# Kernel tuning notes

Measured on AMD Instinct MI355X. Metric: run time of the kernel, lower is better.

The kernel has to match this reference:

```python
import jax, jax.numpy as jnp
import numpy as np

B, S, D = 4, 1024, 512          # batch, seq, d_model
F, DF = 16, 64                  # raw feature dim, d_feat_emb
E, H = 8, 1024                  # n_experts (4 groups x scale 2), expert hidden
DFF = 2048                      # shared FFN hidden = max(round(d_ff*1.0), d_model)
K = 2                           # top_k
TEMP = 1.0                      # router temperature
EPS = 1e-5                      # layer_norm_eps


def _ln(x, g, b):
    m = jnp.mean(x, axis=-1, keepdims=True)
    v = jnp.mean(jnp.square(x - m), axis=-1, keepdims=True)
    return (x - m) * jax.lax.rsqrt(v + EPS) * g + b


def setup_inputs() -> dict:
    key = jax.random.key(0)
    ks = jax.random.split(key, 16)

    def w(k, shape, fan_in):
        return jax.random.normal(k, shape, dtype=jnp.float32) * (1.0 / np.sqrt(fan_in))

    return {
        "hidden_states": jax.random.normal(ks[0], (B, S, D), dtype=jnp.float32),
        "stage_raw_feat": jax.random.normal(ks[1], (B, S, F), dtype=jnp.float32),
        "ln_g": jnp.ones((D,), jnp.float32),
        "ln_b": jnp.zeros((D,), jnp.float32),
        "pre_ln_g": jnp.ones((D,), jnp.float32),
        "pre_ln_b": jnp.zeros((D,), jnp.float32),
        "feat_w": w(ks[2], (F, DF), F),
        "feat_b": jnp.zeros((DF,), jnp.float32),
        "film_w": w(ks[3], (DF, 2 * D), DF),
        "film_b": jnp.zeros((2 * D,), jnp.float32),
        "router_w": w(ks[4], (D, E), D),
        "router_b": jnp.zeros((E,), jnp.float32),
        "w1": w(ks[5], (E, D, H), D),
        "b1": jnp.zeros((E, H), jnp.float32),
        "w2": w(ks[6], (E, H, D), H),
        "b2": jnp.zeros((E, D), jnp.float32),
        "fc1_w": w(ks[7], (D, DFF), D),
        "fc1_b": jnp.zeros((DFF,), jnp.float32),
        "fc2_w": w(ks[8], (DFF, D), DFF),
        "fc2_b": jnp.zeros((D,), jnp.float32),
        "alpha": jnp.float32(0.5),
    }


def reference(hidden_states, stage_raw_feat, ln_g, ln_b, pre_ln_g, pre_ln_b,
              feat_w, feat_b, film_w, film_b, router_w, router_b,
              w1, b1, w2, b2, fc1_w, fc1_b, fc2_w, fc2_b, alpha):
    # Pre-MoE LayerNorm
    x = _ln(hidden_states, ln_g, ln_b)                       # [B,S,D]

    # Feature encoder + FiLM injection of stage features into expert input
    feat = stage_raw_feat @ feat_w + feat_b                  # [B,S,DF]
    film = feat @ film_w + film_b                            # [B,S,2D]
    gamma, beta = jnp.split(film, 2, axis=-1)
    x_in = x * (1.0 + gamma) + beta                          # [B,S,D]

    # Token-level learned router (source='hidden'), top-k softmax over picked logits
    logits = (x @ router_w + router_b) / TEMP                # [B,S,E]
    top_vals, top_idx = jax.lax.top_k(logits, K)             # [B,S,K]
    gates = jax.nn.softmax(top_vals, axis=-1)                # [B,S,K]
    gate_full = (jax.nn.one_hot(top_idx, E, dtype=x.dtype) * gates[..., None]).sum(-2)  # [B,S,E]

    # Expert MLPs (depth=1): dense all-expert compute, sparse gate combine
    h = jax.nn.gelu(jnp.einsum('bsd,edh->bseh', x_in, w1) + b1)          # [B,S,E,H]
    moe = jnp.einsum('bseh,ehd,bse->bsd', h, w2, gate_full)
    moe = moe + jnp.einsum('bse,ed->bsd', gate_full, b2)                 # [B,S,D]

    # Shared FFN residual branch (shared_moe_learned)
    xs = _ln(hidden_states, pre_ln_g, pre_ln_b)
    shared = jax.nn.gelu(xs @ fc1_w + fc1_b) @ fc2_w + fc2_b             # [B,S,D]

    return hidden_states + shared + alpha * moe
```

## Files before the change

### kernel.cpp

```cpp
#include <hip/hip_runtime.h>
#include <hip/hip_bf16.h>

typedef __attribute__((ext_vector_type(8))) short short8;
typedef __attribute__((ext_vector_type(4))) float f32x4;
typedef unsigned short u16;

#define TTOK 4096
#define DMOD 512
#define DFFN 2048
#define NEXP 8
#define HEXP 1024

__device__ __forceinline__ u16 to_bf16(float f) {
    union { __hip_bfloat16 h; u16 u; } cv;
    cv.h = __float2bfloat16(f);
    return cv.u;
}

__device__ __forceinline__ float gelu_tanh(float x) {
    const float c = 0.7978845608028654f;
    float y = c * (x + 0.044715f * x * x * x);
    return x / (1.0f + __expf(-2.0f * y));
}

__device__ __forceinline__ float4 ld_bf4(const u16* p) {
    ushort4 u = *(const ushort4*)p;
    union { unsigned i; float f; } a, b, c, d;
    a.i = (unsigned)u.x << 16; b.i = (unsigned)u.y << 16;
    c.i = (unsigned)u.z << 16; d.i = (unsigned)u.w << 16;
    return make_float4(a.f, b.f, c.f, d.f);
}

__device__ __forceinline__ void gload16(const u16* g, u16* l) {
    __builtin_amdgcn_global_load_lds(
        (__attribute__((address_space(1))) void*)g,
        (__attribute__((address_space(3))) void*)l, 16, 0, 0);
}

__global__ __launch_bounds__(256) void pack_weights(
    const float* __restrict__ fc1_w, const float* __restrict__ fc2_w,
    const float* __restrict__ w1, const float* __restrict__ w2,
    u16* __restrict__ fc1p, u16* __restrict__ fc2p,
    u16* __restrict__ w1p, u16* __restrict__ w2p)
{
    int t = blockIdx.x * 256 + threadIdx.x;
    const float* src; u16* dst; int N, k, n;
    if (t < 131072) {
        int u = t; int lane = u & 63; int fs = u >> 6; int s = fs & 15;
        int q = lane >> 4, rr = lane & 15;
        src = fc1_w; dst = fc1p + (size_t)u * 8; N = 2048;
        k = s * 32 + q * 8; n = ((fs >> 4) * 16) + rr;
    } else if (t < 262144) {
        int u = t - 131072; int lane = u & 63; int fs = u >> 6; int s = fs & 63;
        int q = lane >> 4, rr = lane & 15;
        src = fc2_w; dst = fc2p + (size_t)u * 8; N = 512;
        k = s * 32 + q * 8; n = ((fs >> 6) * 16) + rr;
    } else if (t < 786432) {
        int u = t - 262144; int e = u >> 16; int v = u & 65535;
        int lane = v & 63; int fs = v >> 6; int s = fs & 15;
        int q = lane >> 4, rr = lane & 15;
        src = w1 + (size_t)e * 524288; dst = w1p + (size_t)u * 8; N = 1024;
        k = s * 32 + q * 8; n = ((fs >> 4) * 16) + rr;
    } else {
        int u = t - 786432; int e = u >> 16; int v = u & 65535;
        int lane = v & 63; int fs = v >> 6; int s = fs & 31;
        int q = lane >> 4, rr = lane & 15;
        src = w2 + (size_t)e * 524288; dst = w2p + (size_t)u * 8; N = 512;
        k = s * 32 + q * 8; n = ((fs >> 5) * 16) + rr;
    }
    u16 ov[8];
#pragma unroll
    for (int j = 0; j < 8; ++j)
        ov[j] = to_bf16(src[(size_t)(k + j) * N + n]);
    *(uint4*)dst = *(uint4*)ov;
}

__global__ __launch_bounds__(256) void ln_kernel(
    const float* __restrict__ hidden, const float* __restrict__ raw,
    const float* __restrict__ ln_g, const float* __restrict__ ln_b,
    const float* __restrict__ pre_g, const float* __restrict__ pre_b,
    const float* __restrict__ feat_w, const float* __restrict__ feat_b,
    const float* __restrict__ router_w, const float* __restrict__ router_b,
    u16* __restrict__ xs, float* __restrict__ xbuf, float* __restrict__ featbuf,
    float* __restrict__ logits)
{
    const int tid = threadIdx.x, lane = tid & 63, w = tid >> 6;
    const int t = blockIdx.x * 4 + w;
    __shared__ float pl8[4][64][8];
    __shared__ float raw_sh[4][16];

    const float* xrow = hidden + (size_t)t * DMOD + lane * 8;
    float4 xa = *(const float4*)(xrow);
    float4 xb = *(const float4*)(xrow + 4);
    if (lane < 16) raw_sh[w][lane] = raw[(size_t)t * 16 + lane];

    float s = xa.x + xa.y + xa.z + xa.w + xb.x + xb.y + xb.z + xb.w;
    float q = xa.x*xa.x + xa.y*xa.y + xa.z*xa.z + xa.w*xa.w
            + xb.x*xb.x + xb.y*xb.y + xb.z*xb.z + xb.w*xb.w;
#pragma unroll
    for (int m = 32; m > 0; m >>= 1) { s += __shfl_xor(s, m); q += __shfl_xor(q, m); }
    float mean = s * (1.0f / 512.0f);
    float var  = q * (1.0f / 512.0f) - mean * mean;
    float rstd = rsqrtf(var + 1e-5f);

    float4 na, nb;
    na.x = (xa.x - mean) * rstd; na.y = (xa.y - mean) * rstd;
    na.z = (xa.z - mean) * rstd; na.w = (xa.w - mean) * rstd;
    nb.x = (xb.x - mean) * rstd; nb.y = (xb.y - mean) * rstd;
    nb.z = (xb.z - mean) * rstd; nb.w = (xb.w - mean) * rstd;

    const int d8 = lane * 8;
    float4 pga = *(const float4*)(pre_g + d8), pgb = *(const float4*)(pre_g + d8 + 4);
    float4 pba = *(const float4*)(pre_b + d8), pbb = *(const float4*)(pre_b + d8 + 4);
    u16 ov[8];
    ov[0] = to_bf16(na.x * pga.x + pba.x); ov[1] = to_bf16(na.y * pga.y + pba.y);
    ov[2] = to_bf16(na.z * pga.z + pba.z); ov[3] = to_bf16(na.w * pga.w + pba.w);
    ov[4] = to_bf16(nb.x * pgb.x + pbb.x); ov[5] = to_bf16(nb.y * pgb.y + pbb.y);
    ov[6] = to_bf16(nb.z * pgb.z + pbb.z); ov[7] = to_bf16(nb.w * pgb.w + pbb.w);
    *(uint4*)(xs + (size_t)t * DMOD + d8) = *(uint4*)ov;

    float4 lga = *(const float4*)(ln_g + d8), lgb = *(const float4*)(ln_g + d8 + 4);
    float4 lba = *(const float4*)(ln_b + d8), lbb = *(const float4*)(ln_b + d8 + 4);
    float4 x03, x47;
    x03.x = na.x * lga.x + lba.x; x03.y = na.y * lga.y + lba.y;
    x03.z = na.z * lga.z + lba.z; x03.w = na.w * lga.w + lba.w;
    x47.x = nb.x * lgb.x + lbb.x; x47.y = nb.y * lgb.y + lbb.y;
    x47.z = nb.z * lgb.z + lbb.z; x47.w = nb.w * lgb.w + lbb.w;
    *(float4*)(xbuf + (size_t)t * DMOD + d8) = x03;
    *(float4*)(xbuf + (size_t)t * DMOD + d8 + 4) = x47;

    float4 p03 = make_float4(0.f, 0.f, 0.f, 0.f), p47 = p03;
    const float* rw = router_w + (size_t)d8 * 8;
#pragma unroll
    for (int j = 0; j < 8; ++j) {
        float xv = (j < 4) ? ((j == 0) ? x03.x : (j == 1) ? x03.y : (j == 2) ? x03.z : x03.w)
                           : ((j == 4) ? x47.x : (j == 5) ? x47.y : (j == 6) ? x47.z : x47.w);
        float4 r0 = *(const float4*)(rw + j * 8);
        float4 r1 = *(const float4*)(rw + j * 8 + 4);
        p03.x += xv * r0.x; p03.y += xv * r0.y; p03.z += xv * r0.z; p03.w += xv * r0.w;
        p47.x += xv * r1.x; p47.y += xv * r1.y; p47.z += xv * r1.z; p47.w += xv * r1.w;
    }
    *(float4*)(&pl8[w][lane][0]) = p03;
    *(float4*)(&pl8[w][lane][4]) = p47;
    if (lane < 8) {
        float acc = router_b[lane];
#pragma unroll 8
        for (int i = 0; i < 64; ++i) acc += pl8[w][i][lane];
        logits[(size_t)t * 8 + lane] = acc;
    }

    float fv = feat_b[lane];
#pragma unroll
    for (int f = 0; f < 16; ++f) fv += raw_sh[w][f] * feat_w[f * 64 + lane];
    featbuf[(size_t)t * 64 + lane] = fv;
}

__global__ __launch_bounds__(256) void bucket_kernel(
    const float* __restrict__ logits, int* __restrict__ cnt, int* __restrict__ slots,
    float* __restrict__ gslot, int* __restrict__ eslot)
{
    const int tid = threadIdx.x;
    const int t = blockIdx.x * 256 + tid;
    __shared__ int csh[8], base[8];
    if (tid < 8) csh[tid] = 0;
    __syncthreads();

    float4 l0 = *(const float4*)(logits + (size_t)t * 8);
    float4 l1 = *(const float4*)(logits + (size_t)t * 8 + 4);
    float v0 = -1e30f, v1 = -1e30f; int i0 = 0, i1 = 0;
#define CK(val, idx) { float v = (val); if (v > v0) { v1 = v0; i1 = i0; v0 = v; i0 = idx; } \
                       else if (v > v1) { v1 = v; i1 = idx; } }
    CK(l0.x, 0) CK(l0.y, 1) CK(l0.z, 2) CK(l0.w, 3)
    CK(l1.x, 4) CK(l1.y, 5) CK(l1.z, 6) CK(l1.w, 7)
#undef CK
    float g1 = 1.0f / (1.0f + __expf(v0 - v1));
    float g0 = 1.0f - g1;
    int r0 = atomicAdd(&csh[i0], 1);
    int r1 = atomicAdd(&csh[i1], 1);
    __syncthreads();
    if (tid < 8) base[tid] = atomicAdd(&cnt[tid], csh[tid]);
    __syncthreads();
    int p0 = base[i0] + r0, p1 = base[i1] + r1;
    slots[i0 * TTOK + p0] = 2 * t;
    slots[i1 * TTOK + p1] = 2 * t + 1;
    gslot[2 * t] = g0;     eslot[2 * t] = i0;
    gslot[2 * t + 1] = g1; eslot[2 * t + 1] = i1;
}

__global__ __launch_bounds__(256) void film_kernel(
    const float* __restrict__ xbuf, const float* __restrict__ featbuf,
    const float* __restrict__ film_w, const float* __restrict__ film_b,
    u16* __restrict__ xin)
{
    const int t0 = blockIdx.x * 8, tid = threadIdx.x;
    __shared__ float fs[8 * 64];
#pragma unroll
    for (int i = 0; i < 2; ++i)
        fs[tid + i * 256] = featbuf[(size_t)t0 * 64 + tid + i * 256];
    __syncthreads();

    float acc[8][4];
#pragma unroll
    for (int t = 0; t < 8; ++t) { acc[t][0] = 0.f; acc[t][1] = 0.f; acc[t][2] = 0.f; acc[t][3] = 0.f; }

    for (int j = 0; j < 64; ++j) {
        const float* fw = film_w + (size_t)j * 1024 + tid;
        float w0 = fw[0], w1 = fw[256], w2 = fw[512], w3 = fw[768];
#pragma unroll
        for (int t = 0; t < 8; ++t) {
            float fv = fs[t * 64 + j];
            acc[t][0] += fv * w0; acc[t][1] += fv * w1;
            acc[t][2] += fv * w2; acc[t][3] += fv * w3;
        }
    }
    float b0 = film_b[tid], b1 = film_b[tid + 256], b2 = film_b[tid + 512], b3 = film_b[tid + 768];
#pragma unroll
    for (int t = 0; t < 8; ++t) {
        size_t row = (size_t)(t0 + t) * DMOD;
        float xv0 = xbuf[row + tid], xv1 = xbuf[row + tid + 256];
        xin[row + tid]       = to_bf16(xv0 * (1.0f + acc[t][0] + b0) + acc[t][2] + b2);
        xin[row + tid + 256] = to_bf16(xv1 * (1.0f + acc[t][1] + b1) + acc[t][3] + b3);
    }
}

template<int KCHUNKS>
__device__ __forceinline__ void gemm32(
    const u16* const rp[8],
    const u16* Bf0, int S, int sbase,
    f32x4 acc[2][4], u16* As)
{
    const int tid = threadIdx.x, lane = tid & 63, w = tid >> 6;
    const int q = lane >> 4, rr = lane & 15, l7 = lane & 7;
#pragma unroll
    for (int mi = 0; mi < 2; ++mi)
#pragma unroll
        for (int nj = 0; nj < 4; ++nj) {
            acc[mi][nj][0] = 0.f; acc[mi][nj][1] = 0.f;
            acc[mi][nj][2] = 0.f; acc[mi][nj][3] = 0.f;
        }
    const u16* Bi[4];
#pragma unroll
    for (int i = 0; i < 4; ++i)
        Bi[i] = Bf0 + ((size_t)i * S + sbase) * 512 + lane * 8;

#pragma unroll
    for (int i = 0; i < 8; ++i)
        gload16(rp[i] + (lane ^ i) * 8, As + (w * 8 + i) * 512);
    __syncthreads();

    short8 bn[4];
#pragma unroll
    for (int i = 0; i < 4; ++i) bn[i] = *(const short8*)(Bi[i]);

    const int a0base = rr * 512, a1base = (16 + rr) * 512;
#pragma unroll
    for (int c = 0; c < KCHUNKS; ++c) {
#pragma unroll
        for (int sl = 0; sl < 16; ++sl) {
            short8 b0 = bn[0], b1 = bn[1], b2 = bn[2], b3 = bn[3];
            int nstep = c * 16 + sl + 1;
            if (nstep < KCHUNKS * 16) {
#pragma unroll
                for (int i = 0; i < 4; ++i)
                    bn[i] = *(const short8*)(Bi[i] + (size_t)nstep * 512);
            }
            int pa = ((sl * 4 + q) ^ l7) * 8;
            short8 a0 = *(const short8*)(As + a0base + pa);
            short8 a1 = *(const short8*)(As + a1base + pa);
            acc[0][0] = __builtin_amdgcn_mfma_f32_16x16x32_bf16(a0, b0, acc[0][0], 0, 0, 0);
            acc[1][0] = __builtin_amdgcn_mfma_f32_16x16x32_bf16(a1, b0, acc[1][0], 0, 0, 0);
            acc[0][1] = __builtin_amdgcn_mfma_f32_16x16x32_bf16(a0, b1, acc[0][1], 0, 0, 0);
            acc[1][1] = __builtin_amdgcn_mfma_f32_16x16x32_bf16(a1, b1, acc[1][1], 0, 0, 0);
            acc[0][2] = __builtin_amdgcn_mfma_f32_16x16x32_bf16(a0, b2, acc[0][2], 0, 0, 0);
            acc[1][2] = __builtin_amdgcn_mfma_f32_16x16x32_bf16(a1, b2, acc[1][2], 0, 0, 0);
            acc[0][3] = __builtin_amdgcn_mfma_f32_16x16x32_bf16(a0, b3, acc[0][3], 0, 0, 0);
            acc[1][3] = __builtin_amdgcn_mfma_f32_16x16x32_bf16(a1, b3, acc[1][3], 0, 0, 0);
        }
        if (c + 1 < KCHUNKS) {
            __syncthreads();
#pragma unroll
            for (int i = 0; i < 8; ++i)
                gload16(rp[i] + (c + 1) * 512 + (lane ^ i) * 8, As + (w * 8 + i) * 512);
            __syncthreads();
        }
    }
}

__global__ __launch_bounds__(256) void stage1_kernel(
    const u16* __restrict__ xs, const u16* __restrict__ fc1p, const float* __restrict__ fc1_b,
    u16* __restrict__ h1,
    const u16* __restrict__ xin, const u16* __restrict__ w1p, const float* __restrict__ b1,
    const int* __restrict__ cnt, const int* __restrict__ slots, u16* __restrict__ hbuf)
{
    __shared__ __align__(16) u16 As[16384];
    const int tid = threadIdx.x, lane = tid & 63, w = tid >> 6;
    const int cb = lane & 15, rq = (lane >> 4) * 4;
    const int m0 = blockIdx.x * 32;
    const u16* rp[8];
    f32x4 acc[2][4];

    if (blockIdx.z == 8) {
        const int f0 = blockIdx.y * 16 + w * 4;
#pragma unroll
        for (int i = 0; i < 8; ++i) rp[i] = xs + (size_t)(m0 + w * 8 + i) * 512;
        gemm32<1>(rp, fc1p + (size_t)f0 * 8192, 16, 0, acc, As);
#pragma unroll
        for (int mi = 0; mi < 2; ++mi)
#pragma unroll
            for (int nj = 0; nj < 4; ++nj) {
                int col = (f0 + nj) * 16 + cb;
                float bias = fc1_b[col];
#pragma unroll
                for (int r = 0; r < 4; ++r) {
                    int row = m0 + mi * 16 + rq + r;
                    h1[(size_t)row * DFFN + col] = to_bf16(gelu_tanh(acc[mi][nj][r] + bias));
                }
            }
    } else {
        if (blockIdx.y >= 4) return;
        const int e = blockIdx.z, ce = cnt[e];
        if (m0 >= ce) return;
        const int* sl = slots + e * TTOK;
        const int f0 = blockIdx.y * 16 + w * 4;
#pragma unroll
        for (int i = 0; i < 8; ++i) {
            int p = m0 + w * 8 + i; if (p > ce - 1) p = ce - 1;
            rp[i] = xin + (size_t)(sl[p] >> 1) * 512;
        }
        gemm32<1>(rp, w1p + (size_t)e * 524288 + (size_t)f0 * 8192, 16, 0, acc, As);
#pragma unroll
        for (int mi = 0; mi < 2; ++mi)
#pragma unroll
            for (int r = 0; r < 4; ++r) {
                int p = m0 + mi * 16 + rq + r;
                if (p < ce) {
                    int slot = sl[p];
#pragma unroll
                    for (int nj = 0; nj < 4; ++nj) {
                        int col = (f0 + nj) * 16 + cb;
                        hbuf[(size_t)slot * HEXP + col] = to_bf16(gelu_tanh(acc[mi][nj][r] + b1[e * HEXP + col]));
                    }
                }
            }
    }
}

__global__ __launch_bounds__(256) void stage2_kernel(
    const u16* __restrict__ h1, const u16* __restrict__ fc2p,
    const u16* __restrict__ hbuf, const u16* __restrict__ w2p,
    const int* __restrict__ cnt, const int* __restrict__ slots,
    u16* __restrict__ pf, u16* __restrict__ pm)
{
    __shared__ __align__(16) u16 As[16384];
    const int tid = threadIdx.x, lane = tid & 63, w = tid >> 6;
    const int cb = lane & 15, rq = (lane >> 4) * 4;
    const int m0 = blockIdx.x * 32;
    const int ks = blockIdx.y & 1, nb = blockIdx.y >> 1;
    const int f0 = nb * 16 + w * 4;
    const u16* rp[8];
    f32x4 acc[2][4];

    if (blockIdx.z == 8) {
#pragma unroll
        for (int i = 0; i < 8; ++i)
            rp[i] = h1 + (size_t)(m0 + w * 8 + i) * DFFN + ks * 1024;
        gemm32<2>(rp, fc2p + (size_t)f0 * 32768, 64, ks * 32, acc, As);
        u16* dst = pf + (size_t)ks * TTOK * DMOD;
#pragma unroll
        for (int mi = 0; mi < 2; ++mi)
#pragma unroll
            for (int nj = 0; nj < 4; ++nj) {
                int col = (f0 + nj) * 16 + cb;
#pragma unroll
                for (int r = 0; r < 4; ++r) {
                    int row = m0 + mi * 16 + rq + r;
                    dst[(size_t)row * DMOD + col] = to_bf16(acc[mi][nj][r]);
                }
            }
    } else {
        const int e = blockIdx.z, ce = cnt[e];
        if (m0 >= ce) return;
        const int* sl = slots + e * TTOK;
#pragma unroll
        for (int i = 0; i < 8; ++i) {
            int p = m0 + w * 8 + i; if (p > ce - 1) p = ce - 1;
            rp[i] = hbuf + (size_t)sl[p] * HEXP + ks * 512;
        }
        gemm32<1>(rp, w2p + (size_t)e * 524288 + (size_t)f0 * 16384, 32, ks * 16, acc, As);
        u16* dst = pm + (size_t)ks * 2 * TTOK * DMOD;
#pragma unroll
        for (int mi = 0; mi < 2; ++mi)
#pragma unroll
            for (int r = 0; r < 4; ++r) {
                int p = m0 + mi * 16 + rq + r;
                if (p < ce) {
                    int slot = sl[p];
#pragma unroll
                    for (int nj = 0; nj < 4; ++nj) {
                        int col = (f0 + nj) * 16 + cb;
                        dst[(size_t)slot * DMOD + col] = to_bf16(acc[mi][nj][r]);
                    }
                }
            }
    }
}

__global__ __launch_bounds__(256) void combine_kernel(
    const float* __restrict__ hidden, const u16* __restrict__ pf, const u16* __restrict__ pm,
    const float* __restrict__ fc2_b, const float* __restrict__ b2,
    const float* __restrict__ gslot, const int* __restrict__ eslot,
    const float* __restrict__ alpha, float* __restrict__ out)
{
    int i = blockIdx.x * 256 + threadIdx.x;
    int t = i >> 7, d = (i & 127) * 4;
    float a = alpha[0];
    float4 h = ((const float4*)hidden)[i];
    float4 bias = *(const float4*)(fc2_b + d);

    size_t fo = (size_t)t * DMOD + d;
    float4 f0 = ld_bf4(pf + fo), f1 = ld_bf4(pf + (size_t)TTOK * DMOD + fo);

    int s0 = 2 * t, s1 = 2 * t + 1;
    float g0 = gslot[s0], g1 = gslot[s1];
    int e0 = eslot[s0], e1 = eslot[s1];
    size_t mo0 = (size_t)s0 * DMOD + d, mo1 = (size_t)s1 * DMOD + d;
    const u16* pm1 = pm + (size_t)2 * TTOK * DMOD;
    float4 ma = ld_bf4(pm + mo0), mb = ld_bf4(pm1 + mo0);
    float4 mc = ld_bf4(pm + mo1), md = ld_bf4(pm1 + mo1);
    float4 ba = *(const float4*)(b2 + e0 * DMOD + d);
    float4 bb = *(const float4*)(b2 + e1 * DMOD + d);

    float4 o;
    o.x = h.x + f0.x + f1.x + bias.x + a * (g0 * (ma.x + mb.x + ba.x) + g1 * (mc.x + md.x + bb.x));
    o.y = h.y + f0.y + f1.y + bias.y + a * (g0 * (ma.y + mb.y + ba.y) + g1 * (mc.y + md.y + bb.y));
    o.z = h.z + f0.z + f1.z + bias.z + a * (g0 * (ma.z + mb.z + ba.z) + g1 * (mc.z + md.z + bb.z));
    o.w = h.w + f0.w + f1.w + bias.w + a * (g0 * (ma.w + mb.w + ba.w) + g1 * (mc.w + md.w + bb.w));
    ((float4*)out)[i] = o;
}

extern "C" void kernel_launch(void* const* d_in, const int* in_sizes, int n_in,
                              void* d_out, int out_size, void* d_ws, size_t ws_size,
                              hipStream_t stream)
{
    const float* hidden   = (const float*)d_in[0];
    const float* raw      = (const float*)d_in[1];
    const float* ln_g     = (const float*)d_in[2];
    const float* ln_b     = (const float*)d_in[3];
    const float* pre_g    = (const float*)d_in[4];
    const float* pre_b    = (const float*)d_in[5];
    const float* feat_w   = (const float*)d_in[6];
    const float* feat_b   = (const float*)d_in[7];
    const float* film_w   = (const float*)d_in[8];
    const float* film_b   = (const float*)d_in[9];
    const float* router_w = (const float*)d_in[10];
    const float* router_b = (const float*)d_in[11];
    const float* w1       = (const float*)d_in[12];
    const float* b1       = (const float*)d_in[13];
    const float* w2       = (const float*)d_in[14];
    const float* b2       = (const float*)d_in[15];
    const float* fc1_w    = (const float*)d_in[16];
    const float* fc1_b    = (const float*)d_in[17];
    const float* fc2_w    = (const float*)d_in[18];
    const float* fc2_b    = (const float*)d_in[19];
    const float* alpha    = (const float*)d_in[20];
    float* out = (float*)d_out;

    char* w = (char*)d_ws;
    auto alloc = [&](size_t b) { char* p = w; w += (b + 255) & ~(size_t)255; return p; };
    u16*  fc1p = (u16*)alloc((size_t)DFFN * DMOD * 2);
    u16*  fc2p = (u16*)alloc((size_t)DMOD * DFFN * 2);
    u16*  w1p  = (u16*)alloc((size_t)NEXP * HEXP * DMOD * 2);
    u16*  w2p  = (u16*)alloc((size_t)NEXP * DMOD * HEXP * 2);
    u16*  xs   = (u16*)alloc((size_t)TTOK * DMOD * 2);
    u16*  xin  = (u16*)alloc((size_t)TTOK * DMOD * 2);
    u16*  h1   = (u16*)alloc((size_t)TTOK * DFFN * 2);
    u16*  hb   = (u16*)alloc((size_t)2 * TTOK * HEXP * 2);
    u16*  pf   = (u16*)alloc((size_t)2 * TTOK * DMOD * 2);
    u16*  pm   = (u16*)alloc((size_t)2 * 2 * TTOK * DMOD * 2);
    int*   cnt   = (int*)alloc(NEXP * 4);
    int*   slots = (int*)alloc((size_t)NEXP * TTOK * 4);
    float* gslot = (float*)alloc((size_t)2 * TTOK * 4);
    int*   eslot = (int*)alloc((size_t)2 * TTOK * 4);
    float* logits = (float*)alloc((size_t)TTOK * 8 * 4);
    float* xbuf  = (float*)pm;
    float* featbuf = (float*)h1;

    hipMemsetAsync(cnt, 0, NEXP * 4, stream);
    pack_weights<<<5120, 256, 0, stream>>>(fc1_w, fc2_w, w1, w2, fc1p, fc2p, w1p, w2p);
    ln_kernel<<<1024, 256, 0, stream>>>(hidden, raw, ln_g, ln_b, pre_g, pre_b,
        feat_w, feat_b, router_w, router_b, xs, xbuf, featbuf, logits);
    bucket_kernel<<<16, 256, 0, stream>>>(logits, cnt, slots, gslot, eslot);
    film_kernel<<<512, 256, 0, stream>>>(xbuf, featbuf, film_w, film_b, xin);
    stage1_kernel<<<dim3(128, 8, 9), 256, 0, stream>>>(xs, fc1p, fc1_b, h1,
        xin, w1p, b1, cnt, slots, hb);
    stage2_kernel<<<dim3(128, 4, 9), 256, 0, stream>>>(h1, fc2p, hb, w2p, cnt, slots, pf, pm);
    combine_kernel<<<2048, 256, 0, stream>>>(hidden, pf, pm, fc2_b, b2, gslot, eslot, alpha, out);
}
```

Before: 252.5 us.

## Enlarge GEMM M-tile to 64 rows with double-buffered B fragments

Replaces the 32-row GEMM tile with a 64-row tile, so each block does 16 MFMAs per step and every B fragment loaded from global memory is reused across four A sub-tiles instead of two. A is now staged in 256-wide K chunks with a new XOR swizzle that is applied in the global load addresses, and B fragments are prefetched two steps ahead in a ping-pong register buffer. The grid's M dimension is halved to match. This cuts weight traffic per output but raises register pressure from 64 accumulator floats and yields fewer blocks, so occupancy and tail efficiency may drop, especially for sparse experts.

```diff
diff --git a/kernel.cpp b/kernel.cpp
--- a/kernel.cpp
+++ b/kernel.cpp
@@ -223,64 +223,78 @@
     }
 }
 
-template<int KCHUNKS>
-__device__ __forceinline__ void gemm32(
+template<int NSTEPS>
+__device__ __forceinline__ void gemm64(
     const u16* const rp[8],
     const u16* Bf0, int S, int sbase,
-    f32x4 acc[2][4], u16* As)
+    f32x4 acc[4][4], u16* As)
 {
     const int tid = threadIdx.x, lane = tid & 63, w = tid >> 6;
-    const int q = lane >> 4, rr = lane & 15, l7 = lane & 7;
-#pragma unroll
-    for (int mi = 0; mi < 2; ++mi)
+    const int q = lane >> 4, rr = lane & 15;
+#pragma unroll
+    for (int mi = 0; mi < 4; ++mi)
 #pragma unroll
         for (int nj = 0; nj < 4; ++nj) {
             acc[mi][nj][0] = 0.f; acc[mi][nj][1] = 0.f;
             acc[mi][nj][2] = 0.f; acc[mi][nj][3] = 0.f;
         }
-    const u16* Bi[4];
+    const u16* Bn[4];
 #pragma unroll
     for (int i = 0; i < 4; ++i)
-        Bi[i] = Bf0 + ((size_t)i * S + sbase) * 512 + lane * 8;
-
-#pragma unroll
-    for (int i = 0; i < 8; ++i)
-        gload16(rp[i] + (lane ^ i) * 8, As + (w * 8 + i) * 512);
+        Bn[i] = Bf0 + ((size_t)i * S + sbase) * 512 + lane * 8;
+
+#pragma unroll
+    for (int j = 0; j < 8; ++j)
+        gload16(rp[j], As + (w * 16 + 2 * j) * 256);
+
+    short8 bb[2][4];
+#pragma unroll
+    for (int i = 0; i < 4; ++i) { bb[0][i] = *(const short8*)(Bn[i]); }
+#pragma unroll
+    for (int i = 0; i < 4; ++i) { bb[1][i] = *(const short8*)(Bn[i] + 512); Bn[i] += 1024; }
     __syncthreads();
 
-    short8 bn[4];
-#pragma unroll
-    for (int i = 0; i < 4; ++i) bn[i] = *(const short8*)(Bi[i]);
-
-    const int a0base = rr * 512, a1base = (16 + rr) * 512;
-#pragma unroll
-    for (int c = 0; c < KCHUNKS; ++c) {
-#pragma unroll
-        for (int sl = 0; sl < 16; ++sl) {
-            short8 b0 = bn[0], b1 = bn[1], b2 = bn[2], b3 = bn[3];
-            int nstep = c * 16 + sl + 1;
-            if (nstep < KCHUNKS * 16) {
-#pragma unroll
-                for (int i = 0; i < 4; ++i)
-                    bn[i] = *(const short8*)(Bi[i] + (size_t)nstep * 512);
+    constexpr int NCH = NSTEPS / 8;
+    const int ab0 = rr * 256, ab1 = (16 + rr) * 256, ab2 = (32 + rr) * 256, ab3 = (48 + rr) * 256;
+#pragma unroll 1
+    for (int c = 0; c < NCH; ++c) {
+#pragma unroll
+        for (int sl = 0; sl < 8; ++sl) {
+            short8 b0 = bb[sl & 1][0], b1 = bb[sl & 1][1];
+            short8 b2 = bb[sl & 1][2], b3 = bb[sl & 1][3];
+            if (c * 8 + sl + 2 < NSTEPS) {
+#pragma unroll
+                for (int i = 0; i < 4; ++i) bb[sl & 1][i] = *(const short8*)(Bn[i]);
             }
-            int pa = ((sl * 4 + q) ^ l7) * 8;
-            short8 a0 = *(const short8*)(As + a0base + pa);
-            short8 a1 = *(const short8*)(As + a1base + pa);
+#pragma unroll
+            for (int i = 0; i < 4; ++i) Bn[i] += 512;
+            int pa = (((sl * 4 + q) ^ rr) & 31) * 8;
+            short8 a0 = *(const short8*)(As + ab0 + pa);
+            short8 a1 = *(const short8*)(As + ab1 + (pa ^ 128));
+            short8 a2 = *(const short8*)(As + ab2 + pa);
+            short8 a3 = *(const short8*)(As + ab3 + (pa ^ 128));
             acc[0][0] = __builtin_amdgcn_mfma_f32_16x16x32_bf16(a0, b0, acc[0][0], 0, 0, 0);
             acc[1][0] = __builtin_amdgcn_mfma_f32_16x16x32_bf16(a1, b0, acc[1][0], 0, 0, 0);
+            acc[2][0] = __builtin_amdgcn_mfma_f32_16x16x32_bf16(a2, b0, acc[2][0], 0, 0, 0);
+            acc[3][0] = __builtin_amdgcn_mfma_f32_16x16x32_bf16(a3, b0, acc[3][0], 0, 0, 0);
             acc[0][1] = __builtin_amdgcn_mfma_f32_16x16x32_bf16(a0, b1, acc[0][1], 0, 0, 0);
             acc[1][1] = __builtin_amdgcn_mfma_f32_16x16x32_bf16(a1, b1, acc[1][1], 0, 0, 0);
+            acc[2][1] = __builtin_amdgcn_mfma_f32_16x16x32_bf16(a2, b1, acc[2][1], 0, 0, 0);
+            acc[3][1] = __builtin_amdgcn_mfma_f32_16x16x32_bf16(a3, b1, acc[3][1], 0, 0, 0);
             acc[0][2] = __builtin_amdgcn_mfma_f32_16x16x32_bf16(a0, b2, acc[0][2], 0, 0, 0);
             acc[1][2] = __builtin_amdgcn_mfma_f32_16x16x32_bf16(a1, b2, acc[1][2], 0, 0, 0);
+            acc[2][2] = __builtin_amdgcn_mfma_f32_16x16x32_bf16(a2, b2, acc[2][2], 0, 0, 0);
+            acc[3][2] = __builtin_amdgcn_mfma_f32_16x16x32_bf16(a3, b2, acc[3][2], 0, 0, 0);
             acc[0][3] = __builtin_amdgcn_mfma_f32_16x16x32_bf16(a0, b3, acc[0][3], 0, 0, 0);
             acc[1][3] = __builtin_amdgcn_mfma_f32_16x16x32_bf16(a1, b3, acc[1][3], 0, 0, 0);
-        }
-        if (c + 1 < KCHUNKS) {
+            acc[2][3] = __builtin_amdgcn_mfma_f32_16x16x32_bf16(a2, b3, acc[2][3], 0, 0, 0);
+            acc[3][3] = __builtin_amdgcn_mfma_f32_16x16x32_bf16(a3, b3, acc[3][3], 0, 0, 0);
+        }
+        if (c + 1 < NCH) {
             __syncthreads();
 #pragma unroll
-            for (int i = 0; i < 8; ++i)
-                gload16(rp[i] + (c + 1) * 512 + (lane ^ i) * 8, As + (w * 8 + i) * 512);
+            for (int j = 0; j < 8; ++j)
+                gload16(rp[j] + (c + 1) * 256, As + (w * 16 + 2 * j) * 256);
             __syncthreads();
         }
     }
@@ -295,17 +309,21 @@
     __shared__ __align__(16) u16 As[16384];
     const int tid = threadIdx.x, lane = tid & 63, w = tid >> 6;
     const int cb = lane & 15, rq = (lane >> 4) * 4;
-    const int m0 = blockIdx.x * 32;
+    const int m0 = blockIdx.x * 64;
+    const int l31 = lane & 31, lh = lane >> 5;
+    const int f0 = blockIdx.y * 16 + w * 4;
     const u16* rp[8];
-    f32x4 acc[2][4];
+    f32x4 acc[4][4];
 
     if (blockIdx.z == 8) {
-        const int f0 = blockIdx.y * 16 + w * 4;
-#pragma unroll
-        for (int i = 0; i < 8; ++i) rp[i] = xs + (size_t)(m0 + w * 8 + i) * 512;
-        gemm32<1>(rp, fc1p + (size_t)f0 * 8192, 16, 0, acc, As);
-#pragma unroll
-        for (int mi = 0; mi < 2; ++mi)
+#pragma unroll
+        for (int j = 0; j < 8; ++j) {
+            int ri = w * 16 + 2 * j + lh;
+            rp[j] = xs + (size_t)(m0 + ri) * 512 + ((l31 ^ (ri & 31)) * 8);
+        }
+        gemm64<16>(rp, fc1p + (size_t)f0 * 8192, 16, 0, acc, As);
+#pragma unroll
+        for (int mi = 0; mi < 4; ++mi)
 #pragma unroll
             for (int nj = 0; nj < 4; ++nj) {
                 int col = (f0 + nj) * 16 + cb;
@@ -321,15 +339,15 @@
         const int e = blockIdx.z, ce = cnt[e];
         if (m0 >= ce) return;
         const int* sl = slots + e * TTOK;
-        const int f0 = blockIdx.y * 16 + w * 4;
-#pragma unroll
-        for (int i = 0; i < 8; ++i) {
-            int p = m0 + w * 8 + i; if (p > ce - 1) p = ce - 1;
-            rp[i] = xin + (size_t)(sl[p] >> 1) * 512;
-        }
-        gemm32<1>(rp, w1p + (size_t)e * 524288 + (size_t)f0 * 8192, 16, 0, acc, As);
-#pragma unroll
-        for (int mi = 0; mi < 2; ++mi)
+#pragma unroll
+        for (int j = 0; j < 8; ++j) {
+            int ri = w * 16 + 2 * j + lh;
+            int p = m0 + ri; if (p > ce - 1) p = ce - 1;
+            rp[j] = xin + (size_t)(sl[p] >> 1) * 512 + ((l31 ^ (ri & 31)) * 8);
+        }
+        gemm64<16>(rp, w1p + (size_t)e * 524288 + (size_t)f0 * 8192, 16, 0, acc, As);
+#pragma unroll
+        for (int mi = 0; mi < 4; ++mi)
 #pragma unroll
             for (int r = 0; r < 4; ++r) {
                 int p = m0 + mi * 16 + rq + r;
@@ -354,20 +372,23 @@
     __shared__ __align__(16) u16 As[16384];
     const int tid = threadIdx.x, lane = tid & 63, w = tid >> 6;
     const int cb = lane & 15, rq = (lane >> 4) * 4;
-    const int m0 = blockIdx.x * 32;
+    const int m0 = blockIdx.x * 64;
+    const int l31 = lane & 31, lh = lane >> 5;
     const int ks = blockIdx.y & 1, nb = blockIdx.y >> 1;
     const int f0 = nb * 16 + w * 4;
     const u16* rp[8];
-    f32x4 acc[2][4];
+    f32x4 acc[4][4];
 
     if (blockIdx.z == 8) {
 #pragma unroll
-        for (int i = 0; i < 8; ++i)
-            rp[i] = h1 + (size_t)(m0 + w * 8 + i) * DFFN + ks * 1024;
-        gemm32<2>(rp, fc2p + (size_t)f0 * 32768, 64, ks * 32, acc, As);
+        for (int j = 0; j < 8; ++j) {
+            int ri = w * 16 + 2 * j + lh;
+            rp[j] = h1 + (size_t)(m0 + ri) * DFFN + ks * 1024 + ((l31 ^ (ri & 31)) * 8);
+        }
+        gemm64<32>(rp, fc2p + (size_t)f0 * 32768, 64, ks * 32, acc, As);
         u16* dst = pf + (size_t)ks * TTOK * DMOD;
 #pragma unroll
-        for (int mi = 0; mi < 2; ++mi)
+        for (int mi = 0; mi < 4; ++mi)
 #pragma unroll
             for (int nj = 0; nj < 4; ++nj) {
                 int col = (f0 + nj) * 16 + cb;
@@ -382,14 +403,15 @@
         if (m0 >= ce) return;
         const int* sl = slots + e * TTOK;
 #pragma unroll
-        for (int i = 0; i < 8; ++i) {
-            int p = m0 + w * 8 + i; if (p > ce - 1) p = ce - 1;
-            rp[i] = hbuf + (size_t)sl[p] * HEXP + ks * 512;
-        }
-        gemm32<1>(rp, w2p + (size_t)e * 524288 + (size_t)f0 * 16384, 32, ks * 16, acc, As);
+        for (int j = 0; j < 8; ++j) {
+            int ri = w * 16 + 2 * j + lh;
+            int p = m0 + ri; if (p > ce - 1) p = ce - 1;
+            rp[j] = hbuf + (size_t)sl[p] * HEXP + ks * 512 + ((l31 ^ (ri & 31)) * 8);
+        }
+        gemm64<16>(rp, w2p + (size_t)e * 524288 + (size_t)f0 * 16384, 32, ks * 16, acc, As);
         u16* dst = pm + (size_t)ks * 2 * TTOK * DMOD;
 #pragma unroll
-        for (int mi = 0; mi < 2; ++mi)
+        for (int mi = 0; mi < 4; ++mi)
 #pragma unroll
             for (int r = 0; r < 4; ++r) {
                 int p = m0 + mi * 16 + rq + r;
@@ -491,8 +513,8 @@
         feat_w, feat_b, router_w, router_b, xs, xbuf, featbuf, logits);
     bucket_kernel<<<16, 256, 0, stream>>>(logits, cnt, slots, gslot, eslot);
     film_kernel<<<512, 256, 0, stream>>>(xbuf, featbuf, film_w, film_b, xin);
-    stage1_kernel<<<dim3(128, 8, 9), 256, 0, stream>>>(xs, fc1p, fc1_b, h1,
+    stage1_kernel<<<dim3(64, 8, 9), 256, 0, stream>>>(xs, fc1p, fc1_b, h1,
         xin, w1p, b1, cnt, slots, hb);
-    stage2_kernel<<<dim3(128, 4, 9), 256, 0, stream>>>(h1, fc2p, hb, w2p, cnt, slots, pf, pm);
+    stage2_kernel<<<dim3(64, 4, 9), 256, 0, stream>>>(h1, fc2p, hb, w2p, cnt, slots, pf, pm);
     combine_kernel<<<2048, 256, 0, stream>>>(hidden, pf, pm, fc2_b, b2, gslot, eslot, alpha, out);
 }
```

Measured after the change: 277.0 us. +9.7%, slower.
